# Performance work log

Hardware: AMD Instinct MI355X
Metric: run time of the kernel (lower is better)

Reference implementation:

```python
import jax, jax.numpy as jnp
import numpy as np

B, S, D = 4, 2048, 2048
H = 16
DH = D // H  # 128


def setup_inputs() -> dict:
    key = jax.random.key(0)
    ks = jax.random.split(key, 12)
    s = 1.0 / np.sqrt(D)
    inp = {
        "Q": jax.random.normal(ks[0], (B, S, D), jnp.float32),
        "K": jax.random.normal(ks[1], (B, S, D), jnp.float32),
        "V": jax.random.normal(ks[2], (B, S, D), jnp.float32),
        "mask": jnp.tril(jnp.ones((S, S), jnp.int32))[None, None],  # causal [1,1,S,S]
        "wq": jax.random.uniform(ks[3], (D, D), jnp.float32, -s, s),
        "bq": jax.random.uniform(ks[4], (D,), jnp.float32, -s, s),
        "wk": jax.random.uniform(ks[5], (D, D), jnp.float32, -s, s),
        "bk": jax.random.uniform(ks[6], (D,), jnp.float32, -s, s),
        "wv": jax.random.uniform(ks[7], (D, D), jnp.float32, -s, s),
        "bv": jax.random.uniform(ks[8], (D,), jnp.float32, -s, s),
        "wo": jax.random.uniform(ks[9], (D, D), jnp.float32, -s, s),
        "bo": jax.random.uniform(ks[10], (D,), jnp.float32, -s, s),
    }
    return inp


def _split_heads(x):
    # [B,S,D] -> [B,H,S,DH]
    b, s, _ = x.shape
    return x.reshape(b, s, H, DH).transpose(0, 2, 1, 3)


def reference(Q, K, V, mask, wq, bq, wk, bk, wv, bv, wo, bo):
    q = _split_heads(Q @ wq + bq)
    k = _split_heads(K @ wk + bk)
    v = _split_heads(V @ wv + bv)
    scores = jnp.einsum("bhqd,bhkd->bhqk", q, k) / jnp.sqrt(jnp.float32(DH))
    scores = jnp.where(mask == 0, jnp.float32(-1e9), scores)
    probs = jax.nn.softmax(scores, axis=-1)
    attn = jnp.einsum("bhqk,bhkd->bhqd", probs, v)  # [B,H,S,DH]
    attn = attn.transpose(0, 2, 1, 3).reshape(Q.shape[0], Q.shape[1], D)
    return attn @ wo + bo
```

## Files before the change

kernel.cpp:

```cpp
#include <hip/hip_runtime.h>
#include <hip/hip_bf16.h>

typedef __attribute__((ext_vector_type(8))) short short8;
typedef __attribute__((ext_vector_type(4))) float f32x4;

#define DEVINL __device__ __forceinline__

constexpr int Bc = 4, Sc = 2048, Dc = 2048, Hc = 16, DHc = 128;
constexpr float SCALE2 = 0.08838834764831845f * 1.4426950408889634f;

DEVINL float exp2s(float x) { return __builtin_amdgcn_exp2f(x); }

DEVINL short f2bf(float f) {
  unsigned u = __builtin_bit_cast(unsigned, f);
  u = (u + 0x7fffu + ((u >> 16) & 1u)) >> 16;
  return (short)u;
}
DEVINL unsigned pack2(float a, float b) {
  return (unsigned)(unsigned short)f2bf(a) | ((unsigned)(unsigned short)f2bf(b) << 16);
}

DEVINL void gload16(const void* g, void* l) {
  __builtin_amdgcn_global_load_lds(
      (const __attribute__((address_space(1))) void*)g,
      (__attribute__((address_space(3))) void*)l, 16, 0, 0);
}

__global__ __launch_bounds__(256) void transpose_w_kernel(
    const float* __restrict__ w0, const float* __restrict__ w1,
    const float* __restrict__ w2, const float* __restrict__ w3,
    short* __restrict__ wt) {
  __shared__ float tile[32][33];
  const float* w = (blockIdx.z == 0) ? w0 : (blockIdx.z == 1) ? w1
                   : (blockIdx.z == 2) ? w2 : w3;
  short* out = wt + (size_t)blockIdx.z * Dc * Dc;
  int k0 = blockIdx.x * 32, n0 = blockIdx.y * 32;
  int t = threadIdx.x;
#pragma unroll
  for (int p = 0; p < 4; ++p) {
    int idx = p * 256 + t;
    int kr = idx >> 5, nc = idx & 31;
    tile[kr][nc] = w[(size_t)(k0 + kr) * Dc + n0 + nc];
  }
  __syncthreads();
#pragma unroll
  for (int p = 0; p < 4; ++p) {
    int idx = p * 256 + t;
    int nr = idx >> 5, kc = idx & 31;
    out[(size_t)(n0 + nr) * Dc + k0 + kc] = f2bf(tile[kc][nr]);
  }
}

__global__ __launch_bounds__(256) void convert_kernel(
    const float* __restrict__ in, short* __restrict__ out, int n8) {
  int stride = gridDim.x * 256;
  for (int idx = blockIdx.x * 256 + threadIdx.x; idx < n8; idx += stride) {
    const f32x4* p = (const f32x4*)(in + (size_t)idx * 8);
    f32x4 a = p[0], b = p[1];
    short8 r;
    r[0] = f2bf(a[0]); r[1] = f2bf(a[1]); r[2] = f2bf(a[2]); r[3] = f2bf(a[3]);
    r[4] = f2bf(b[0]); r[5] = f2bf(b[1]); r[6] = f2bf(b[2]); r[7] = f2bf(b[3]);
    *(short8*)(out + (size_t)idx * 8) = r;
  }
}

template <int OUT_MODE>
__global__ __launch_bounds__(512, 1) void gemm_ring_kernel(
    const short* __restrict__ A, const short* __restrict__ Wt,
    const float* __restrict__ bias, void* __restrict__ Cptr) {
  __shared__ __align__(16) short As[4][256 * 32];
  __shared__ __align__(16) short Bs[4][256 * 32];
  const int tid = threadIdx.x, lane = tid & 63, wid = tid >> 6;
  const int wm = wid >> 2, wn = wid & 3;
  const int lr = lane & 15, g = lane >> 4;
  const int physg = (g ^ ((lr >> 1) & 3)) * 8;

  const int bid = blockIdx.x;
  const int swz = (bid & 7) * 32 + (bid >> 3);
  const int m0 = (swz >> 3) * 256, n0 = (swz & 7) * 256;

  const int srow = lane >> 2;
  const int scol = ((lane & 3) ^ ((lane >> 3) & 3)) * 8;
  const size_t abase = (size_t)(m0 + wid * 32 + srow) * Dc + scol;
  const size_t bbase = (size_t)(n0 + wid * 32 + srow) * Dc + scol;
  const int ldof = wid * 32 * 64;

  auto stageA = [&](int kt) {
    const short* src = &A[abase + kt * 32];
    char* dst = (char*)&As[kt & 3][0] + ldof;
    gload16(src, dst);
    gload16(src + (size_t)16 * Dc, dst + 16 * 64);
  };
  auto stageB = [&](int kt) {
    const short* src = &Wt[bbase + kt * 32];
    char* dst = (char*)&Bs[kt & 3][0] + ldof;
    gload16(src, dst);
    gload16(src + (size_t)16 * Dc, dst + 16 * 64);
  };

  f32x4 acc[8][4] = {};

  stageA(0); stageB(0);
  stageA(1); stageB(1);
  stageA(2); stageB(2);

  for (int kt = 0; kt < 64; ++kt) {
    if (kt < 62) {
      asm volatile("s_waitcnt vmcnt(8)" ::: "memory");
    } else if (kt == 62) {
      asm volatile("s_waitcnt vmcnt(4)" ::: "memory");
    } else {
      asm volatile("s_waitcnt vmcnt(0)" ::: "memory");
    }
    __builtin_amdgcn_s_barrier();
    asm volatile("" ::: "memory");

    const short* Ab = &As[kt & 3][0];
    const short* Bb = &Bs[kt & 3][0];
    short8 afr[4], bfr[4], af2[4];
#pragma unroll
    for (int i = 0; i < 4; ++i)
      afr[i] = *(const short8*)&Ab[(wm * 128 + i * 16 + lr) * 32 + physg];
#pragma unroll
    for (int j = 0; j < 4; ++j)
      bfr[j] = *(const short8*)&Bb[(wn * 64 + j * 16 + lr) * 32 + physg];
#pragma unroll
    for (int i = 0; i < 4; ++i)
      af2[i] = *(const short8*)&Ab[(wm * 128 + 64 + i * 16 + lr) * 32 + physg];

    if (kt <= 60) { stageA(kt + 3); stageB(kt + 3); }

    __builtin_amdgcn_s_setprio(1);
#pragma unroll
    for (int i = 0; i < 4; ++i)
#pragma unroll
      for (int j = 0; j < 4; ++j)
        acc[i][j] = __builtin_amdgcn_mfma_f32_16x16x32_bf16(afr[i], bfr[j], acc[i][j], 0, 0, 0);
#pragma unroll
    for (int i = 0; i < 4; ++i)
#pragma unroll
      for (int j = 0; j < 4; ++j)
        acc[4 + i][j] = __builtin_amdgcn_mfma_f32_16x16x32_bf16(af2[i], bfr[j], acc[4 + i][j], 0, 0, 0);
    __builtin_amdgcn_s_setprio(0);
  }

  const int rowl = g * 4;
#pragma unroll
  for (int bj = 0; bj < 4; ++bj) {
    const int gcol = n0 + wn * 64 + bj * 16 + lr;
    const float bv = bias[gcol];
#pragma unroll
    for (int ai = 0; ai < 8; ++ai) {
#pragma unroll
      for (int r = 0; r < 4; ++r) {
        int grow = m0 + wm * 128 + ai * 16 + rowl + r;
        float v = acc[ai][bj][r] + bv;
        if (OUT_MODE == 1) {
          ((float*)Cptr)[(size_t)grow * Dc + gcol] = v;
        } else if (OUT_MODE == 0) {
          ((short*)Cptr)[(size_t)grow * Dc + gcol] = f2bf(v);
        } else {
          int b4 = grow >> 11, ss = grow & (Sc - 1);
          int hh = gcol >> 7, dh = gcol & (DHc - 1);
          ((short*)Cptr)[((((size_t)(b4 * Hc + hh) * DHc) + dh) << 11) + ss] = f2bf(v);
        }
      }
    }
  }
}

__global__ __launch_bounds__(512, 2) void attn_kernel(
    const short* __restrict__ qp, const short* __restrict__ kp,
    const short* __restrict__ vt, short* __restrict__ attn) {
  __shared__ __align__(16) short Ks[64 * 128];
  __shared__ __align__(16) short Vs[128 * 64];
  __shared__ __align__(16) short Ps[8][32][72];
  const int tid = threadIdx.x, lane = tid & 63, wid = tid >> 6;
  const int lr = lane & 15, g = lane >> 4, lk = g * 8, rowl = g * 4;
  const int d = blockIdx.x;
  const int xcd = d & 7, s = d >> 3;
  const int grp = s >> 3;
  const int qi = (grp < 4) ? grp : 11 - grp;
  const int bh = xcd * 8 + (s & 7);
  const int b = bh >> 4, h = bh & 15;
  const int qb = qi * 256;
  const size_t headq = ((size_t)b * Sc) * Dc + (size_t)h * DHc;
  const size_t vbase = (((size_t)b * Hc + h) * DHc) << 11;
  const int qw = qb + wid * 32;
  const int x7 = lr & 7;

  short8 qf[2][4];
#pragma unroll
  for (int qs = 0; qs < 2; ++qs)
#pragma unroll
    for (int c = 0; c < 4; ++c)
      qf[qs][c] = *(const short8*)&qp[headq + (size_t)(qw + qs * 16 + lr) * Dc + c * 32 + lk];

  const int krow = wid * 4 + g;
  const int kcol = lr * 8;
  const int vrow = wid * 8 + (lane >> 3);
  const int vcol = (lane & 7) * 8;
  int kdst[2], vdst[2];
#pragma unroll
  for (int p = 0; p < 2; ++p) {
    int kr = p * 32 + krow;
    kdst[p] = kr * 128 + ((lr ^ (kr & 7)) * 8);
    int vr = p * 64 + vrow;
    vdst[p] = vr * 64 + (((lane & 7) ^ (vr & 7)) * 8);
  }

  short8 kreg[2], vreg[2];
  auto issue = [&](int kvb) {
#pragma unroll
    for (int p = 0; p < 2; ++p)
      kreg[p] = *(const short8*)&kp[headq + (size_t)(kvb + p * 32 + krow) * Dc + kcol];
#pragma unroll
    for (int p = 0; p < 2; ++p)
      vreg[p] = *(const short8*)&vt[vbase + (size_t)(p * 64 + vrow) * Sc + kvb + vcol];
  };
  auto commit = [&]() {
#pragma unroll
    for (int p = 0; p < 2; ++p) *(short8*)&Ks[kdst[p]] = kreg[p];
#pragma unroll
    for (int p = 0; p < 2; ++p) *(short8*)&Vs[vdst[p]] = vreg[p];
  };

  issue(0);
  commit();
  __syncthreads();

  f32x4 o[2][8] = {};
  float mrun[2] = {-1e30f, -1e30f}, lrun[2] = {0.f, 0.f};
  const int ntiles = qb / 64 + 4;

  for (int t = 0; t < ntiles; ++t) {
    const bool active = (64 * t <= qw + 31);
    f32x4 sc[2][4];

    if (active) {
      __builtin_amdgcn_s_setprio(1);
#pragma unroll
      for (int nb = 0; nb < 4; ++nb) {
        f32x4 s0 = {}, s1 = {};
#pragma unroll
        for (int c = 0; c < 4; ++c) {
          short8 kf = *(const short8*)&Ks[(nb * 16 + lr) * 128 + (((c * 4 + g) ^ x7) << 3)];
          s0 = __builtin_amdgcn_mfma_f32_16x16x32_bf16(kf, qf[0][c], s0, 0, 0, 0);
          s1 = __builtin_amdgcn_mfma_f32_16x16x32_bf16(kf, qf[1][c], s1, 0, 0, 0);
        }
        sc[0][nb] = s0;
        sc[1][nb] = s1;
      }
      __builtin_amdgcn_s_setprio(0);
    }

    if (t + 1 < ntiles) issue((t + 1) * 64);

    if (active) {
      const bool domask = (64 * t + 63 > qw);
#pragma unroll
      for (int qs = 0; qs < 2; ++qs) {
        const int qg = qw + qs * 16 + lr;
        float mnb[4];
#pragma unroll
        for (int nb = 0; nb < 4; ++nb) {
#pragma unroll
          for (int r = 0; r < 4; ++r) {
            float v = sc[qs][nb][r] * SCALE2;
            if (domask) {
              int kv = t * 64 + nb * 16 + rowl + r;
              v = (kv > qg) ? -1e30f : v;
            }
            sc[qs][nb][r] = v;
          }
          mnb[nb] = fmaxf(fmaxf(sc[qs][nb][0], sc[qs][nb][1]),
                          fmaxf(sc[qs][nb][2], sc[qs][nb][3]));
        }
        float mt = fmaxf(fmaxf(mnb[0], mnb[1]), fmaxf(mnb[2], mnb[3]));
        mt = fmaxf(mt, __shfl_xor(mt, 16));
        mt = fmaxf(mt, __shfl_xor(mt, 32));

        float mnew = fmaxf(mrun[qs], mt);
        float alpha = exp2s(mrun[qs] - mnew);
        mrun[qs] = mnew;

        float lsnb[4];
#pragma unroll
        for (int nb = 0; nb < 4; ++nb) {
          float p0 = exp2s(sc[qs][nb][0] - mnew);
          float p1 = exp2s(sc[qs][nb][1] - mnew);
          float p2 = exp2s(sc[qs][nb][2] - mnew);
          float p3 = exp2s(sc[qs][nb][3] - mnew);
          lsnb[nb] = (p0 + p1) + (p2 + p3);
          uint2 w;
          w.x = pack2(p0, p1);
          w.y = pack2(p2, p3);
          *(uint2*)&Ps[wid][qs * 16 + lr][nb * 16 + rowl] = w;
        }
        float ls = (lsnb[0] + lsnb[1]) + (lsnb[2] + lsnb[3]);
        ls += __shfl_xor(ls, 16);
        ls += __shfl_xor(ls, 32);
        lrun[qs] = lrun[qs] * alpha + ls;

        float al[4];
#pragma unroll
        for (int r = 0; r < 4; ++r) al[r] = __shfl(alpha, (lane & 48) | (rowl + r));
#pragma unroll
        for (int f = 0; f < 8; ++f)
#pragma unroll
          for (int r = 0; r < 4; ++r) o[qs][f][r] *= al[r];
      }

      asm volatile("s_waitcnt lgkmcnt(0)" ::: "memory");
      __builtin_amdgcn_sched_barrier(0);

      __builtin_amdgcn_s_setprio(1);
#pragma unroll
      for (int kc = 0; kc < 2; ++kc) {
        short8 pf0 = *(const short8*)&Ps[wid][lr][kc * 32 + lk];
        short8 pf1 = *(const short8*)&Ps[wid][16 + lr][kc * 32 + lk];
#pragma unroll
        for (int nb = 0; nb < 8; ++nb) {
          short8 vf = *(const short8*)&Vs[(nb * 16 + lr) * 64 + (((kc * 4 + g) ^ x7) << 3)];
          o[0][nb] = __builtin_amdgcn_mfma_f32_16x16x32_bf16(pf0, vf, o[0][nb], 0, 0, 0);
          o[1][nb] = __builtin_amdgcn_mfma_f32_16x16x32_bf16(pf1, vf, o[1][nb], 0, 0, 0);
        }
      }
      __builtin_amdgcn_s_setprio(0);
    }

    __syncthreads();
    if (t + 1 < ntiles) commit();
    __syncthreads();
  }

#pragma unroll
  for (int qs = 0; qs < 2; ++qs) {
    float ld[4];
#pragma unroll
    for (int r = 0; r < 4; ++r) ld[r] = __shfl(lrun[qs], (lane & 48) | (rowl + r));
#pragma unroll
    for (int f = 0; f < 8; ++f)
#pragma unroll
      for (int r = 0; r < 4; ++r) {
        float v = o[qs][f][r] / ld[r];
        attn[headq + (size_t)(qw + qs * 16 + rowl + r) * Dc + f * 16 + lr] = f2bf(v);
      }
  }
}

extern "C" void kernel_launch(void* const* d_in, const int* in_sizes, int n_in,
                              void* d_out, int out_size, void* d_ws, size_t ws_size,
                              hipStream_t stream) {
  const float* Q = (const float*)d_in[0];
  const float* K = (const float*)d_in[1];
  const float* V = (const float*)d_in[2];
  const float* wq = (const float*)d_in[4];
  const float* bq = (const float*)d_in[5];
  const float* wk = (const float*)d_in[6];
  const float* bk = (const float*)d_in[7];
  const float* wv = (const float*)d_in[8];
  const float* bv = (const float*)d_in[9];
  const float* wo = (const float*)d_in[10];
  const float* bo = (const float*)d_in[11];

  char* ws = (char*)d_ws;
  const size_t WSZ = (size_t)Dc * Dc;
  const size_t XSZ = (size_t)Bc * Sc * Dc;
  short* WT = (short*)ws;
  short* QP = (short*)(ws + 4 * WSZ * 2);
  short* KP = (short*)(ws + 4 * WSZ * 2 + XSZ * 2);
  short* VT = (short*)(ws + 4 * WSZ * 2 + 2 * XSZ * 2);
  short* AT = (short*)(ws + 4 * WSZ * 2 + 3 * XSZ * 2);

  transpose_w_kernel<<<dim3(Dc / 32, Dc / 32, 4), 256, 0, stream>>>(wq, wk, wv, wo, WT);

  const int n8 = (int)(XSZ / 8);
  const int ng = (Bc * Sc / 256) * (Dc / 256);

  convert_kernel<<<2048, 256, 0, stream>>>(Q, AT, n8);
  gemm_ring_kernel<0><<<ng, 512, 0, stream>>>(AT, WT, bq, QP);
  convert_kernel<<<2048, 256, 0, stream>>>(K, AT, n8);
  gemm_ring_kernel<0><<<ng, 512, 0, stream>>>(AT, WT + WSZ, bk, KP);
  convert_kernel<<<2048, 256, 0, stream>>>(V, AT, n8);
  gemm_ring_kernel<2><<<ng, 512, 0, stream>>>(AT, WT + 2 * WSZ, bv, VT);

  attn_kernel<<<512, 512, 0, stream>>>(QP, KP, VT, AT);

  gemm_ring_kernel<1><<<ng, 512, 0, stream>>>(AT, WT + 3 * WSZ, bo, (float*)d_out);
}
```

Before: 475.3 us.

## Fuse fp32-to-bf16 input conversion into projection GEMMs and add lazy softmax rescaling

Removes the three separate convert kernels by having a new GEMM variant load fp32 activations into registers, pack them to bf16 and write them into the LDS ring buffer. This drops a full read/write pass of the converted activations per projection. The softmax scale is folded into the Q projection output, so the attention loop no longer multiplies scores. The online-softmax rescale of the output accumulator and running sum is skipped unless the tile max exceeds the running max by more than 8 (log2 units). The fused load path adds register pressure and VALU packing inside the GEMM main loop, and the lazy rescale relies on a bounded drift in the exponent.

```diff
diff --git a/kernel.cpp b/kernel.cpp
--- a/kernel.cpp
+++ b/kernel.cpp
@@ -51,16 +51,132 @@
   }
 }
 
-__global__ __launch_bounds__(256) void convert_kernel(
-    const float* __restrict__ in, short* __restrict__ out, int n8) {
-  int stride = gridDim.x * 256;
-  for (int idx = blockIdx.x * 256 + threadIdx.x; idx < n8; idx += stride) {
-    const f32x4* p = (const f32x4*)(in + (size_t)idx * 8);
-    f32x4 a = p[0], b = p[1];
-    short8 r;
-    r[0] = f2bf(a[0]); r[1] = f2bf(a[1]); r[2] = f2bf(a[2]); r[3] = f2bf(a[3]);
-    r[4] = f2bf(b[0]); r[5] = f2bf(b[1]); r[6] = f2bf(b[2]); r[7] = f2bf(b[3]);
-    *(short8*)(out + (size_t)idx * 8) = r;
+template <int OUT_MODE>
+__global__ __launch_bounds__(512, 1) void gemm_ring_f32_kernel(
+    const float* __restrict__ A, const short* __restrict__ Wt,
+    const float* __restrict__ bias, void* __restrict__ Cptr, float oscale) {
+  __shared__ __align__(16) short As[4][256 * 32];
+  __shared__ __align__(16) short Bs[4][256 * 32];
+  const int tid = threadIdx.x, lane = tid & 63, wid = tid >> 6;
+  const int wm = wid >> 2, wn = wid & 3;
+  const int lr = lane & 15, g = lane >> 4;
+  const int physg = (g ^ ((lr >> 1) & 3)) * 8;
+
+  const int bid = blockIdx.x;
+  const int swz = (bid & 7) * 32 + (bid >> 3);
+  const int m0 = (swz >> 3) * 256, n0 = (swz & 7) * 256;
+
+  const int srow = lane >> 2;
+  const int scol = ((lane & 3) ^ ((lane >> 3) & 3)) * 8;
+  const size_t bbase = (size_t)(n0 + wid * 32 + srow) * Dc + scol;
+  const int ldof = wid * 32 * 64;
+  auto stageB = [&](int kt) {
+    const short* src = &Wt[bbase + kt * 32];
+    char* dst = (char*)&Bs[kt & 3][0] + ldof;
+    gload16(src, dst);
+    gload16(src + (size_t)16 * Dc, dst + 16 * 64);
+  };
+
+  const int arl = wid * 32 + (lane >> 1);
+  const int s0 = (lane & 1) * 2;
+  const size_t afbase = (size_t)(m0 + arl) * Dc + s0 * 8;
+  const int aw0 = arl * 64 + ((s0 ^ ((arl >> 1) & 3)) * 16);
+  const int aw1 = arl * 64 + (((s0 + 1) ^ ((arl >> 1) & 3)) * 16);
+
+  f32x4 areg[4];
+  auto issueA = [&](int kt) {
+    const float* src = &A[afbase + kt * 32];
+    areg[0] = *(const f32x4*)(src);
+    areg[1] = *(const f32x4*)(src + 4);
+    areg[2] = *(const f32x4*)(src + 8);
+    areg[3] = *(const f32x4*)(src + 12);
+  };
+  auto commitA = [&](int kt) {
+    uint4 q0, q1;
+    q0.x = pack2(areg[0][0], areg[0][1]);
+    q0.y = pack2(areg[0][2], areg[0][3]);
+    q0.z = pack2(areg[1][0], areg[1][1]);
+    q0.w = pack2(areg[1][2], areg[1][3]);
+    q1.x = pack2(areg[2][0], areg[2][1]);
+    q1.y = pack2(areg[2][2], areg[2][3]);
+    q1.z = pack2(areg[3][0], areg[3][1]);
+    q1.w = pack2(areg[3][2], areg[3][3]);
+    char* base = (char*)&As[kt & 3][0];
+    *(uint4*)(base + aw0) = q0;
+    *(uint4*)(base + aw1) = q1;
+  };
+
+  f32x4 acc[8][4] = {};
+
+  issueA(0);
+  asm volatile("s_waitcnt vmcnt(0)" ::: "memory");
+  commitA(0); issueA(1); stageB(0);
+  asm volatile("s_waitcnt vmcnt(2)" ::: "memory");
+  commitA(1); issueA(2); stageB(1);
+  asm volatile("s_waitcnt vmcnt(2)" ::: "memory");
+  commitA(2); issueA(3); stageB(2);
+
+  for (int kt = 0; kt < 64; ++kt) {
+    asm volatile("s_waitcnt lgkmcnt(0)" ::: "memory");
+    __builtin_amdgcn_s_barrier();
+    asm volatile("" ::: "memory");
+
+    const short* Ab = &As[kt & 3][0];
+    const short* Bb = &Bs[kt & 3][0];
+    short8 afr[4], bfr[4], af2[4];
+#pragma unroll
+    for (int i = 0; i < 4; ++i)
+      afr[i] = *(const short8*)&Ab[(wm * 128 + i * 16 + lr) * 32 + physg];
+#pragma unroll
+    for (int j = 0; j < 4; ++j)
+      bfr[j] = *(const short8*)&Bb[(wn * 64 + j * 16 + lr) * 32 + physg];
+#pragma unroll
+    for (int i = 0; i < 4; ++i)
+      af2[i] = *(const short8*)&Ab[(wm * 128 + 64 + i * 16 + lr) * 32 + physg];
+
+    if (kt < 62) {
+      asm volatile("s_waitcnt vmcnt(2)" ::: "memory");
+    } else if (kt == 62) {
+      asm volatile("s_waitcnt vmcnt(0)" ::: "memory");
+    }
+    if (kt <= 60) commitA(kt + 3);
+    if (kt <= 59) issueA(kt + 4);
+    if (kt <= 60) stageB(kt + 3);
+
+    __builtin_amdgcn_s_setprio(1);
+#pragma unroll
+    for (int i = 0; i < 4; ++i)
+#pragma unroll
+      for (int j = 0; j < 4; ++j)
+        acc[i][j] = __builtin_amdgcn_mfma_f32_16x16x32_bf16(afr[i], bfr[j], acc[i][j], 0, 0, 0);
+#pragma unroll
+    for (int i = 0; i < 4; ++i)
+#pragma unroll
+      for (int j = 0; j < 4; ++j)
+        acc[4 + i][j] = __builtin_amdgcn_mfma_f32_16x16x32_bf16(af2[i], bfr[j], acc[4 + i][j], 0, 0, 0);
+    __builtin_amdgcn_s_setprio(0);
+  }
+
+  const int rowl = g * 4;
+#pragma unroll
+  for (int bj = 0; bj < 4; ++bj) {
+    const int gcol = n0 + wn * 64 + bj * 16 + lr;
+    const float bv = bias[gcol];
+#pragma unroll
+    for (int ai = 0; ai < 8; ++ai) {
+#pragma unroll
+      for (int r = 0; r < 4; ++r) {
+        int grow = m0 + wm * 128 + ai * 16 + rowl + r;
+        float v = (acc[ai][bj][r] + bv) * oscale;
+        if (OUT_MODE == 0) {
+          ((short*)Cptr)[(size_t)grow * Dc + gcol] = f2bf(v);
+        } else {
+          int b4 = grow >> 11, ss = grow & (Sc - 1);
+          int hh = gcol >> 7, dh = gcol & (DHc - 1);
+          ((short*)Cptr)[((((size_t)(b4 * Hc + hh) * DHc) + dh) << 11) + ss] = f2bf(v);
+        }
+      }
+    }
   }
 }
 
@@ -155,15 +271,7 @@
       for (int r = 0; r < 4; ++r) {
         int grow = m0 + wm * 128 + ai * 16 + rowl + r;
         float v = acc[ai][bj][r] + bv;
-        if (OUT_MODE == 1) {
-          ((float*)Cptr)[(size_t)grow * Dc + gcol] = v;
-        } else if (OUT_MODE == 0) {
-          ((short*)Cptr)[(size_t)grow * Dc + gcol] = f2bf(v);
-        } else {
-          int b4 = grow >> 11, ss = grow & (Sc - 1);
-          int hh = gcol >> 7, dh = gcol & (DHc - 1);
-          ((short*)Cptr)[((((size_t)(b4 * Hc + hh) * DHc) + dh) << 11) + ss] = f2bf(v);
-        }
+        ((float*)Cptr)[(size_t)grow * Dc + gcol] = v;
       }
     }
   }
@@ -264,14 +372,12 @@
         float mnb[4];
 #pragma unroll
         for (int nb = 0; nb < 4; ++nb) {
-#pragma unroll
-          for (int r = 0; r < 4; ++r) {
-            float v = sc[qs][nb][r] * SCALE2;
-            if (domask) {
+          if (domask) {
+#pragma unroll
+            for (int r = 0; r < 4; ++r) {
               int kv = t * 64 + nb * 16 + rowl + r;
-              v = (kv > qg) ? -1e30f : v;
+              if (kv > qg) sc[qs][nb][r] = -1e30f;
             }
-            sc[qs][nb][r] = v;
           }
           mnb[nb] = fmaxf(fmaxf(sc[qs][nb][0], sc[qs][nb][1]),
                           fmaxf(sc[qs][nb][2], sc[qs][nb][3]));
@@ -280,17 +386,28 @@
         mt = fmaxf(mt, __shfl_xor(mt, 16));
         mt = fmaxf(mt, __shfl_xor(mt, 32));
 
-        float mnew = fmaxf(mrun[qs], mt);
-        float alpha = exp2s(mrun[qs] - mnew);
-        mrun[qs] = mnew;
+        if (!__all(mt <= mrun[qs] + 8.f)) {
+          float mnew = fmaxf(mrun[qs], mt);
+          float alpha = exp2s(mrun[qs] - mnew);
+          mrun[qs] = mnew;
+          lrun[qs] *= alpha;
+          float al[4];
+#pragma unroll
+          for (int r = 0; r < 4; ++r) al[r] = __shfl(alpha, (lane & 48) | (rowl + r));
+#pragma unroll
+          for (int f = 0; f < 8; ++f)
+#pragma unroll
+            for (int r = 0; r < 4; ++r) o[qs][f][r] *= al[r];
+        }
+        const float mcur = mrun[qs];
 
         float lsnb[4];
 #pragma unroll
         for (int nb = 0; nb < 4; ++nb) {
-          float p0 = exp2s(sc[qs][nb][0] - mnew);
-          float p1 = exp2s(sc[qs][nb][1] - mnew);
-          float p2 = exp2s(sc[qs][nb][2] - mnew);
-          float p3 = exp2s(sc[qs][nb][3] - mnew);
+          float p0 = exp2s(sc[qs][nb][0] - mcur);
+          float p1 = exp2s(sc[qs][nb][1] - mcur);
+          float p2 = exp2s(sc[qs][nb][2] - mcur);
+          float p3 = exp2s(sc[qs][nb][3] - mcur);
           lsnb[nb] = (p0 + p1) + (p2 + p3);
           uint2 w;
           w.x = pack2(p0, p1);
@@ -300,15 +417,7 @@
         float ls = (lsnb[0] + lsnb[1]) + (lsnb[2] + lsnb[3]);
         ls += __shfl_xor(ls, 16);
         ls += __shfl_xor(ls, 32);
-        lrun[qs] = lrun[qs] * alpha + ls;
-
-        float al[4];
-#pragma unroll
-        for (int r = 0; r < 4; ++r) al[r] = __shfl(alpha, (lane & 48) | (rowl + r));
-#pragma unroll
-        for (int f = 0; f < 8; ++f)
-#pragma unroll
-          for (int r = 0; r < 4; ++r) o[qs][f][r] *= al[r];
+        lrun[qs] += ls;
       }
 
       asm volatile("s_waitcnt lgkmcnt(0)" ::: "memory");
@@ -375,15 +484,11 @@
 
   transpose_w_kernel<<<dim3(Dc / 32, Dc / 32, 4), 256, 0, stream>>>(wq, wk, wv, wo, WT);
 
-  const int n8 = (int)(XSZ / 8);
   const int ng = (Bc * Sc / 256) * (Dc / 256);
 
-  convert_kernel<<<2048, 256, 0, stream>>>(Q, AT, n8);
-  gemm_ring_kernel<0><<<ng, 512, 0, stream>>>(AT, WT, bq, QP);
-  convert_kernel<<<2048, 256, 0, stream>>>(K, AT, n8);
-  gemm_ring_kernel<0><<<ng, 512, 0, stream>>>(AT, WT + WSZ, bk, KP);
-  convert_kernel<<<2048, 256, 0, stream>>>(V, AT, n8);
-  gemm_ring_kernel<2><<<ng, 512, 0, stream>>>(AT, WT + 2 * WSZ, bv, VT);
+  gemm_ring_f32_kernel<0><<<ng, 512, 0, stream>>>(Q, WT, bq, QP, SCALE2);
+  gemm_ring_f32_kernel<0><<<ng, 512, 0, stream>>>(K, WT + WSZ, bk, KP, 1.f);
+  gemm_ring_f32_kernel<2><<<ng, 512, 0, stream>>>(V, WT + 2 * WSZ, bv, VT, 1.f);
 
   attn_kernel<<<512, 512, 0, stream>>>(QP, KP, VT, AT);
 
```

After: 479.5 us. About the same (+0.9%).
